# Kernel tuning notes

Hardware: AMD Instinct MI355X
Metric: run time of the kernel (lower is better)

The kernel has to match this reference:

```python
import jax, jax.numpy as jnp
import numpy as np
import math

B, S, D = 4, 1024, 1024
H, DK = 16, 64
NUM_BUCKETS, MAX_DIST = 32, 128


def _relative_position_bucket(relative_position, num_buckets=NUM_BUCKETS, max_distance=MAX_DIST):
    # bidirectional bucketing (T5 encoder style)
    num_buckets = num_buckets // 2
    buckets = (relative_position > 0).astype(jnp.int32) * num_buckets
    rp = jnp.abs(relative_position)
    max_exact = num_buckets // 2
    is_small = rp < max_exact
    # clamp to >=1 to avoid log(0); masked out by is_small anyway
    rp_large = max_exact + (
        jnp.log(jnp.maximum(rp, 1).astype(jnp.float32) / max_exact)
        / math.log(max_distance / max_exact)
        * (num_buckets - max_exact)
    ).astype(jnp.int32)
    rp_large = jnp.minimum(rp_large, num_buckets - 1)
    return buckets + jnp.where(is_small, rp, rp_large)


def compute_bias(rel_bias_table, q_len, k_len):
    ctx = jnp.arange(q_len)[:, None]
    mem = jnp.arange(k_len)[None, :]
    buckets = _relative_position_bucket(mem - ctx)  # [q,k]
    values = rel_bias_table[buckets]  # [q,k,H]
    return jnp.transpose(values, (2, 0, 1))  # [H,q,k]


def setup_inputs() -> dict:
    key = jax.random.key(0)
    ks = jax.random.split(key, 6)
    return {
        "hidden_states": jax.random.normal(ks[0], (B, S, D), dtype=jnp.float32),
        "Wq": jax.random.normal(ks[1], (D, H * DK), dtype=jnp.float32) * 0.02,
        "Wk": jax.random.normal(ks[2], (D, H * DK), dtype=jnp.float32) * 0.02,
        "Wv": jax.random.normal(ks[3], (D, H * DK), dtype=jnp.float32) * 0.02,
        "Wo": jax.random.normal(ks[4], (H * DK, D), dtype=jnp.float32) * 0.02,
        "rel_bias_table": jax.random.normal(ks[5], (NUM_BUCKETS, H), dtype=jnp.float32),
    }


def reference(hidden_states, Wq, Wk, Wv, Wo, rel_bias_table):
    b, s, _ = hidden_states.shape
    # projections (no bias), split heads -> [b,h,s,dk]
    def heads(x):
        return jnp.transpose(x.reshape(b, s, H, DK), (0, 2, 1, 3))
    q = heads(hidden_states @ Wq)
    k = heads(hidden_states @ Wk)
    v = heads(hidden_states @ Wv)
    # NOTE: T5 attention is UNSCALED (no 1/sqrt(dk))
    scores = jnp.einsum("bhqd,bhkd->bhqk", q, k)
    bias = compute_bias(rel_bias_table, s, s)[None]  # [1,H,s,s]
    scores = scores + bias
    attn = jax.nn.softmax(scores.astype(jnp.float32), axis=-1).astype(scores.dtype)
    out = jnp.einsum("bhqk,bhkd->bhqd", attn, v)
    out = jnp.transpose(out, (0, 2, 1, 3)).reshape(b, s, H * DK)
    return out @ Wo
```

## Files before the change

### kernel.cpp

```cpp
#include <hip/hip_runtime.h>
#include <hip/hip_bf16.h>

typedef __attribute__((ext_vector_type(8))) short short8;
typedef __attribute__((ext_vector_type(4))) float f32x4;
typedef __attribute__((ext_vector_type(4))) unsigned u32x4;
typedef unsigned short u16;

#define AS1 __attribute__((address_space(1)))
#define AS3 __attribute__((address_space(3)))

#define LOG2E 1.44269504088896f
#define FOLD_M 46.166241308446828f
#define EXP2(x) __builtin_amdgcn_exp2f(x)
#define WAITV(n) asm volatile("s_waitcnt vmcnt(" #n ")" ::: "memory")

__device__ __forceinline__ u16 f2bf(float f) {
    unsigned u = __builtin_bit_cast(unsigned, f);
    u += 0x7FFFu + ((u >> 16) & 1u);
    return (u16)(u >> 16);
}

__device__ __forceinline__ unsigned pk2(float a, float b) {
    unsigned ua = __builtin_bit_cast(unsigned, a) + 0x8000u;
    unsigned ub = __builtin_bit_cast(unsigned, b) + 0x8000u;
    return __builtin_amdgcn_perm(ub, ua, 0x07060302);
}

__global__ __launch_bounds__(256) void k_prep(const float* __restrict__ hidden,
                                              const float* __restrict__ Wq, const float* __restrict__ Wk,
                                              const float* __restrict__ Wv, const float* __restrict__ Wo,
                                              const float* __restrict__ tbl,
                                              u16* __restrict__ hidb,
                                              u16* __restrict__ wt, u16* __restrict__ wot,
                                              float* __restrict__ bias2) {
    int z = blockIdx.z;
    if (z >= 5) {
        int i = ((z - 5) * 1024 + blockIdx.y * 32 + blockIdx.x) * 256 + threadIdx.x;
        float4 v = ((const float4*)hidden)[i];
        ushort4 o;
        o.x = f2bf(v.x); o.y = f2bf(v.y); o.z = f2bf(v.z); o.w = f2bf(v.w);
        ((ushort4*)hidb)[i] = o;
        return;
    }
    if (z == 4) {
        int idx = (blockIdx.y * 32 + blockIdx.x) * 256 + threadIdx.x;
        if (idx < 16 * 2048) {
            int r = idx & 2047, h = idx >> 11;
            int rel = r - 1023;
            int bucket = rel > 0 ? 16 : 0;
            int rp = rel < 0 ? -rel : rel;
            if (rp < 8) bucket += rp;
            else {
                int lb = 8 + (int)(log2f((float)rp * 0.125f) * 2.0f);
                bucket += (lb < 15 ? lb : 15);
            }
            bias2[idx] = tbl[bucket * 16 + h] * LOG2E - FOLD_M;
        }
        return;
    }
    const float* in = z == 0 ? Wq : z == 1 ? Wk : z == 2 ? Wv : Wo;
    u16* out = (z == 3) ? wot : wt + (size_t)z * 1024 * 1024;
    __shared__ float tile[32][33];
    int tx = threadIdx.x & 31, ty = threadIdx.x >> 5;
    int bx = blockIdx.x << 5, by = blockIdx.y << 5;
    #pragma unroll
    for (int j = 0; j < 32; j += 8)
        tile[ty + j][tx] = in[(size_t)(by + ty + j) * 1024 + bx + tx];
    __syncthreads();
    #pragma unroll
    for (int j = 0; j < 32; j += 8)
        out[(size_t)(bx + ty + j) * 1024 + by + tx] = f2bf(tile[tx][ty + j]);
}

template<int MODE, int FM>
__global__ __launch_bounds__(256) void k_gemm(const u16* __restrict__ A, const u16* __restrict__ Bt,
                                              u16* __restrict__ oq, u16* __restrict__ ok,
                                              u16* __restrict__ ov, float* __restrict__ outf,
                                              int N) {
    const int K = 1024;
    const int GX = (MODE == 0) ? 24 : 8;
    const int NWG = (MODE == 0) ? 768 : 512;
    __shared__ __align__(16) u16 As[3][FM * 1024];
    __shared__ __align__(16) u16 Bs[3][4096];
    int t = threadIdx.x, lane = t & 63, wave = t >> 6;
    int bid = blockIdx.y * GX + blockIdx.x;
    int sbid = (bid & 7) * (NWG / 8) + (bid >> 3);
    int m0 = (sbid / GX) * (FM * 32), n0 = (sbid % GX) << 7;
    int wm = (wave >> 1) * (FM * 16), wn = (wave & 1) << 6;
    int g = lane >> 4, ln = lane & 15;
    f32x4 acc[FM][4];
    #pragma unroll
    for (int i = 0; i < FM; i++)
        #pragma unroll
        for (int j = 0; j < 4; j++) acc[i][j] = (f32x4){0.f, 0.f, 0.f, 0.f};

    int schunk = ((lane & 3) ^ ((lane >> 3) & 3)) << 3;
    const u16* gA = A + (size_t)(m0 + wave * 16 + (lane >> 2)) * K + schunk;
    const u16* gB = Bt + (size_t)(n0 + wave * 16 + (lane >> 2)) * K + schunk;
    int ldsOff = wave * 512;

    #define GSTAGE(k0_, buf_)                                                                          \
        {                                                                                              \
            u16* sA = &As[buf_][0];                                                                    \
            u16* sB = &Bs[buf_][0];                                                                    \
            __builtin_amdgcn_global_load_lds((const AS1 void*)(gA + (k0_)),                            \
                                             (AS3 void*)&sA[ldsOff], 16, 0, 0);                        \
            if (FM == 4)                                                                               \
                __builtin_amdgcn_global_load_lds((const AS1 void*)(gA + 64 * K + (k0_)),               \
                                                 (AS3 void*)&sA[ldsOff + 2048], 16, 0, 0);             \
            __builtin_amdgcn_global_load_lds((const AS1 void*)(gB + (k0_)),                            \
                                             (AS3 void*)&sB[ldsOff], 16, 0, 0);                        \
            __builtin_amdgcn_global_load_lds((const AS1 void*)(gB + 64 * K + (k0_)),                   \
                                             (AS3 void*)&sB[ldsOff + 2048], 16, 0, 0);                 \
        }

    GSTAGE(0, 0);
    GSTAGE(32, 1);

    int rchunk = (g ^ ((ln >> 1) & 3)) << 3;
    int c0 = 0, c2 = 2;

    for (int kb = 0; kb < 32; kb++) {
        if (kb < 30) {
            GSTAGE((kb + 2) * 32, c2);
            if (FM == 4) WAITV(8); else WAITV(6);
        } else if (kb == 30) {
            if (FM == 4) WAITV(4); else WAITV(3);
        } else {
            WAITV(0);
        }
        __builtin_amdgcn_s_barrier();

        const u16* rA = &As[c0][0];
        const u16* rB = &Bs[c0][0];
        short8 af[FM], bfr[4];
        #pragma unroll
        for (int fm = 0; fm < FM; fm++)
            af[fm] = *(const short8*)&rA[(wm + (fm << 4) + ln) * 32 + rchunk];
        #pragma unroll
        for (int fn = 0; fn < 4; fn++)
            bfr[fn] = *(const short8*)&rB[(wn + (fn << 4) + ln) * 32 + rchunk];
        __builtin_amdgcn_s_setprio(1);
        #pragma unroll
        for (int fm = 0; fm < FM; fm++)
            #pragma unroll
            for (int fn = 0; fn < 4; fn++)
                acc[fm][fn] = __builtin_amdgcn_mfma_f32_16x16x32_bf16(af[fm], bfr[fn], acc[fm][fn], 0, 0, 0);
        __builtin_amdgcn_s_setprio(0);
        __builtin_amdgcn_s_barrier();

        int old = c0;
        c0 = (c0 == 2) ? 0 : c0 + 1;
        c2 = old;
    }

    #pragma unroll
    for (int fm = 0; fm < FM; fm++)
        #pragma unroll
        for (int fn = 0; fn < 4; fn++) {
            int mb = m0 + wm + (fm << 4) + (g << 2);
            int n = n0 + wn + (fn << 4) + ln;
            if (MODE == 0) {
                int j = n >> 10, col = n & 1023;
                int h = col >> 6, dk = col & 63;
                int b = mb >> 10, s = mb & 1023;
                if (j == 2) {
                    ushort4 pk;
                    pk.x = f2bf(acc[fm][fn][0]); pk.y = f2bf(acc[fm][fn][1]);
                    pk.z = f2bf(acc[fm][fn][2]); pk.w = f2bf(acc[fm][fn][3]);
                    *(ushort4*)(ov + ((size_t)(((b << 4) + h) * 64 + dk)) * 1024 + s) = pk;
                } else {
                    u16* dst = (j == 0) ? oq : ok;
                    #pragma unroll
                    for (int r = 0; r < 4; r++)
                        dst[((size_t)(((b << 4) + h) * 1024 + s + r)) * 64 + dk] = f2bf(acc[fm][fn][r]);
                }
            } else {
                #pragma unroll
                for (int r = 0; r < 4; r++)
                    outf[(size_t)(mb + r) * N + n] = acc[fm][fn][r];
            }
        }
    #undef GSTAGE
}

__global__ __launch_bounds__(256, 2) void k_attn(const u16* __restrict__ Qg, const u16* __restrict__ Kg,
                                                 const u16* __restrict__ Vtg, const float* __restrict__ bias2,
                                                 u16* __restrict__ attn_out) {
    __shared__ __align__(16) u16 Ks[2][64 * 64];
    __shared__ __align__(16) u16 Vts[2][64 * 64];
    __shared__ __align__(16) float blds4[4][1160];

    int t = threadIdx.x, lane = t & 63, w = t >> 6;
    int bid = blockIdx.x;
    int sid = (bid & 7) * 64 + (bid >> 3);
    int qb = sid & 7, h = (sid >> 3) & 15, b = sid >> 7;
    int q0 = qb << 7;
    const u16* Qh = Qg + ((size_t)(((b << 4) + h) * 1024 + q0)) * 64;
    const u16* Kh = Kg + (size_t)(((b << 4) + h)) * 1024 * 64;
    const u16* Vth = Vtg + (size_t)(((b << 4) + h)) * 64 * 1024;
    const float* bh = bias2 + (h << 11);

    int g = lane >> 4, ln = lane & 15;
    int lnk = (ln & 3) | ((ln & 4) << 1) | ((ln & 8) >> 1);
    int kbq = ((g & 1) << 3) | ((g >> 1) << 2);

    short8 qf[2][2];
    #pragma unroll
    for (int fm = 0; fm < 2; fm++)
        #pragma unroll
        for (int kh = 0; kh < 2; kh++)
            qf[fm][kh] = *(const short8*)(Qh + (size_t)(w * 32 + fm * 16 + ln) * 64 + kh * 32 + g * 8);

    int w0 = 896 - q0;
    for (int i = t; i < 1152; i += 256) {
        float v = bh[w0 + i];
        #pragma unroll
        for (int a2 = 0; a2 < 4; a2++) { int x = i - a2; if (x >= 0) blds4[a2][x] = v; }
    }
    float b_hi = bh[1023 + 256];
    float b_lo = bh[1023 - 256];
    int aRep = (3 - ln) & 3;
    const float* repB = &blds4[aRep][0];

    #define STAGE(kb_, buf_)                                                                     \
        {                                                                                        \
            _Pragma("unroll")                                                                    \
            for (int r2 = 0; r2 < 2; r2++) {                                                     \
                int L = t * 16 + r2 * 4096;                                                      \
                int row = L >> 7, gI = (L >> 4) & 7, gp = gI ^ (row & 7);                        \
                __builtin_amdgcn_global_load_lds(                                                \
                    (const AS1 void*)(Kh + (size_t)((kb_) * 64 + row) * 64 + gp * 8),            \
                    (AS3 void*)&Ks[buf_][L >> 1], 16, 0, 0);                                     \
                __builtin_amdgcn_global_load_lds(                                                \
                    (const AS1 void*)(Vth + (size_t)row * 1024 + (kb_) * 64 + gp * 8),           \
                    (AS3 void*)&Vts[buf_][L >> 1], 16, 0, 0);                                    \
            }                                                                                    \
        }

    STAGE(0, 0);
    __syncthreads();

    float psum[2] = {0.f, 0.f};
    f32x4 o[2][4];
    #pragma unroll
    for (int fm = 0; fm < 2; fm++)
        #pragma unroll
        for (int dn = 0; dn < 4; dn++) o[fm][dn] = (f32x4){0.f, 0.f, 0.f, 0.f};

    #pragma unroll 2
    for (int kb = 0; kb < 16; kb++) {
        const int cur = kb & 1;
        if (kb < 15) STAGE(kb + 1, cur ^ 1);

        f32x4 s[2][4];
        __builtin_amdgcn_s_setprio(1);
        #pragma unroll
        for (int fn = 0; fn < 4; fn++) {
            int row = (fn << 4) + lnk;
            short8 kf0 = *(const short8*)((const char*)Ks[cur] + row * 128 + (((g << 4) + 0)  ^ ((row & 7) << 4)));
            short8 kf1 = *(const short8*)((const char*)Ks[cur] + row * 128 + (((g << 4) + 64) ^ ((row & 7) << 4)));
            #pragma unroll
            for (int fm = 0; fm < 2; fm++) {
                f32x4 a = (f32x4){0.f, 0.f, 0.f, 0.f};
                a = __builtin_amdgcn_mfma_f32_16x16x32_bf16(kf0, qf[fm][0], a, 0, 0, 0);
                a = __builtin_amdgcn_mfma_f32_16x16x32_bf16(kf1, qf[fm][1], a, 0, 0, 0);
                s[fm][fn] = a;
            }
        }
        __builtin_amdgcn_s_setprio(0);

        int d0 = 64 * kb - q0 - 32 * w;
        int ibase = 64 * kb - 32 * w + 127 + kbq - ln;
        bool fast = (d0 >= 122) || (d0 <= -154);
        float bu = d0 > 0 ? b_hi : b_lo;
        unsigned Px[2][4], Py[2][4];
        #pragma unroll
        for (int fm = 0; fm < 2; fm++)
            #pragma unroll
            for (int fn = 0; fn < 4; fn++) {
                f32x4 sv = s[fm][fn];
                float b0, b1, b2v, b3;
                if (fast) { b0 = b1 = b2v = b3 = bu; }
                else {
                    float4 bb = *(const float4*)(repB + (ibase + 16 * fn - 16 * fm - aRep));
                    b0 = bb.x; b1 = bb.y; b2v = bb.z; b3 = bb.w;
                }
                float p0 = EXP2(fmaf(sv[0], LOG2E, b0));
                float p1 = EXP2(fmaf(sv[1], LOG2E, b1));
                float p2 = EXP2(fmaf(sv[2], LOG2E, b2v));
                float p3 = EXP2(fmaf(sv[3], LOG2E, b3));
                psum[fm] += (p0 + p1) + (p2 + p3);
                Px[fm][fn] = pk2(p0, p1);
                Py[fm][fn] = pk2(p2, p3);
            }

        short8 pa[2][2];
        #pragma unroll
        for (int fm = 0; fm < 2; fm++)
            #pragma unroll
            for (int ks = 0; ks < 2; ks++) {
                unsigned w0r = Px[fm][2 * ks], w2r = Px[fm][2 * ks + 1];
                unsigned w1r = Py[fm][2 * ks], w3r = Py[fm][2 * ks + 1];
                asm volatile("s_nop 1\n\tv_permlane32_swap_b32 %0, %1" : "+v"(w0r), "+v"(w2r));
                asm volatile("s_nop 1\n\tv_permlane32_swap_b32 %0, %1" : "+v"(w1r), "+v"(w3r));
                u32x4 tv; tv[0] = w0r; tv[1] = w1r; tv[2] = w2r; tv[3] = w3r;
                pa[fm][ks] = __builtin_bit_cast(short8, tv);
            }

        __builtin_amdgcn_s_setprio(1);
        #pragma unroll
        for (int dn = 0; dn < 4; dn++) {
            int vrow = (dn << 4) + ln;
            short8 vb0 = *(const short8*)((const char*)Vts[cur] + vrow * 128 + (((g << 4) + 0)  ^ ((vrow & 7) << 4)));
            short8 vb1 = *(const short8*)((const char*)Vts[cur] + vrow * 128 + (((g << 4) + 64) ^ ((vrow & 7) << 4)));
            #pragma unroll
            for (int fm = 0; fm < 2; fm++) {
                f32x4 a = o[fm][dn];
                a = __builtin_amdgcn_mfma_f32_16x16x32_bf16(pa[fm][0], vb0, a, 0, 0, 0);
                a = __builtin_amdgcn_mfma_f32_16x16x32_bf16(pa[fm][1], vb1, a, 0, 0, 0);
                o[fm][dn] = a;
            }
        }
        __builtin_amdgcn_s_setprio(0);

        __syncthreads();
    }

    float linv[2][4];
    #pragma unroll
    for (int fm = 0; fm < 2; fm++) {
        float v = psum[fm];
        v += __shfl_xor(v, 16);
        v += __shfl_xor(v, 32);
        float inv = 1.0f / v;
        #pragma unroll
        for (int r = 0; r < 4; r++)
            linv[fm][r] = __shfl(inv, 4 * g + r);
    }
    #pragma unroll
    for (int fm = 0; fm < 2; fm++)
        #pragma unroll
        for (int dn = 0; dn < 4; dn++)
            #pragma unroll
            for (int r = 0; r < 4; r++) {
                int srow = q0 + 32 * w + 16 * fm + (g << 2) + r;
                int col = (h << 6) + (dn << 4) + ln;
                attn_out[((size_t)((b << 10) + srow) << 10) + col] = f2bf(o[fm][dn][r] * linv[fm][r]);
            }
}

extern "C" void kernel_launch(void* const* d_in, const int* in_sizes, int n_in,
                              void* d_out, int out_size, void* d_ws, size_t ws_size,
                              hipStream_t stream) {
    const float* hidden = (const float*)d_in[0];
    const float* Wq = (const float*)d_in[1];
    const float* Wk = (const float*)d_in[2];
    const float* Wv = (const float*)d_in[3];
    const float* Wo = (const float*)d_in[4];
    const float* tbl = (const float*)d_in[5];

    u16* hidb = (u16*)d_ws;
    u16* wt   = hidb + 4096 * 1024;
    u16* wot  = wt + 3072 * 1024;
    u16* Qb   = wot + 1024 * 1024;
    u16* Kb   = Qb + 4 * 16 * 1024 * 64;
    u16* Vb   = Kb + 4 * 16 * 1024 * 64;
    u16* attn = Vb + 4 * 16 * 1024 * 64;
    float* bias = (float*)(attn + 4096 * 1024);

    k_prep<<<dim3(32, 32, 9), 256, 0, stream>>>(hidden, Wq, Wk, Wv, Wo, tbl, hidb, wt, wot, bias);
    k_gemm<0, 4><<<dim3(24, 32), 256, 0, stream>>>(hidb, wt, Qb, Kb, Vb, nullptr, 3072);
    k_attn<<<512, 256, 0, stream>>>(Qb, Kb, Vb, bias, attn);
    k_gemm<1, 2><<<dim3(8, 64), 256, 0, stream>>>(attn, wot, nullptr, nullptr, nullptr,
                                                  (float*)d_out, 1024);
}
```

Before: 97.24 us.

## Replace QKV projection GEMM with 256x192-tile 512-thread kernel

The fused QKV projection now uses a dedicated kernel with 256x192 output tiles, 8 waves per block, BK=64 double-buffered LDS staging with XOR swizzle, and an XCD-aware tile mapping giving 256 blocks, one per CU. Larger tiles raise arithmetic intensity and cut redundant global/LDS traffic compared with the old 128x128 tile template. The output projection is split into its own non-templated kernel with unchanged behaviour. Risks are higher register pressure from 24 accumulators per wave and a single wave of blocks with no tail balancing.

After: 95.88 us. About the same (-1.4%).

```diff
diff --git a/kernel.cpp b/kernel.cpp
--- a/kernel.cpp
+++ b/kernel.cpp
@@ -72,25 +72,118 @@
         out[(size_t)(bx + ty + j) * 1024 + by + tx] = f2bf(tile[tx][ty + j]);
 }
 
-template<int MODE, int FM>
-__global__ __launch_bounds__(256) void k_gemm(const u16* __restrict__ A, const u16* __restrict__ Bt,
-                                              u16* __restrict__ oq, u16* __restrict__ ok,
-                                              u16* __restrict__ ov, float* __restrict__ outf,
-                                              int N) {
-    const int K = 1024;
-    const int GX = (MODE == 0) ? 24 : 8;
-    const int NWG = (MODE == 0) ? 768 : 512;
-    __shared__ __align__(16) u16 As[3][FM * 1024];
+__global__ __launch_bounds__(512, 2) void k_qkv(const u16* __restrict__ A, const u16* __restrict__ Bt,
+                                                u16* __restrict__ oq, u16* __restrict__ ok,
+                                                u16* __restrict__ ov) {
+    __shared__ __align__(16) u16 As[2][256 * 64];
+    __shared__ __align__(16) u16 Bs[2][192 * 64];
+    int t = threadIdx.x, lane = t & 63, wave = t >> 6;
+    int g = lane >> 4, ln = lane & 15;
+    int wr = wave >> 2, wc = wave & 3;
+
+    int bid = blockIdx.x;
+    int xcd = bid & 7, wgl = bid >> 3;
+    int mt = ((xcd & 3) << 2) + (wgl >> 3);
+    int nt = ((xcd >> 2) << 3) + (wgl & 7);
+    int m0 = mt << 8, n0 = nt * 192;
+
+    f32x4 acc[8][3];
+    #pragma unroll
+    for (int i = 0; i < 8; i++)
+        #pragma unroll
+        for (int j = 0; j < 3; j++) acc[i][j] = (f32x4){0.f, 0.f, 0.f, 0.f};
+
+    #define QSTG(kt_, buf_)                                                                      \
+        {                                                                                        \
+            _Pragma("unroll")                                                                    \
+            for (int u = 0; u < 4; u++) {                                                        \
+                int L = t * 16 + u * 8192;                                                       \
+                int row = L >> 7, gI = (L >> 4) & 7, gp = gI ^ (row & 7);                        \
+                __builtin_amdgcn_global_load_lds(                                                \
+                    (const AS1 void*)(A + (size_t)(m0 + row) * 1024 + (kt_) * 64 + gp * 8),      \
+                    (AS3 void*)&As[buf_][L >> 1], 16, 0, 0);                                     \
+            }                                                                                    \
+            _Pragma("unroll")                                                                    \
+            for (int u = 0; u < 3; u++) {                                                        \
+                int L = t * 16 + u * 8192;                                                       \
+                int row = L >> 7, gI = (L >> 4) & 7, gp = gI ^ (row & 7);                        \
+                __builtin_amdgcn_global_load_lds(                                                \
+                    (const AS1 void*)(Bt + (size_t)(n0 + row) * 1024 + (kt_) * 64 + gp * 8),     \
+                    (AS3 void*)&Bs[buf_][L >> 1], 16, 0, 0);                                     \
+            }                                                                                    \
+        }
+
+    QSTG(0, 0);
+    __syncthreads();
+
+    #pragma unroll 2
+    for (int kt = 0; kt < 16; kt++) {
+        const int c = kt & 1;
+        if (kt < 15) QSTG(kt + 1, c ^ 1);
+
+        #pragma unroll
+        for (int ks = 0; ks < 2; ks++) {
+            short8 af[8], bfr[3];
+            int cb = ((ks << 2) + g) << 4;
+            #pragma unroll
+            for (int mf = 0; mf < 8; mf++) {
+                int row = (wr << 7) + (mf << 4) + ln;
+                af[mf] = *(const short8*)((const char*)&As[c][0] + row * 128 + (cb ^ ((row & 7) << 4)));
+            }
+            #pragma unroll
+            for (int nf = 0; nf < 3; nf++) {
+                int row = wc * 48 + (nf << 4) + ln;
+                bfr[nf] = *(const short8*)((const char*)&Bs[c][0] + row * 128 + (cb ^ ((row & 7) << 4)));
+            }
+            __builtin_amdgcn_s_setprio(1);
+            #pragma unroll
+            for (int mf = 0; mf < 8; mf++)
+                #pragma unroll
+                for (int nf = 0; nf < 3; nf++)
+                    acc[mf][nf] = __builtin_amdgcn_mfma_f32_16x16x32_bf16(af[mf], bfr[nf], acc[mf][nf], 0, 0, 0);
+            __builtin_amdgcn_s_setprio(0);
+        }
+        __syncthreads();
+    }
+    #undef QSTG
+
+    #pragma unroll
+    for (int mf = 0; mf < 8; mf++)
+        #pragma unroll
+        for (int nf = 0; nf < 3; nf++) {
+            int mb = m0 + (wr << 7) + (mf << 4) + (g << 2);
+            int n = n0 + wc * 48 + (nf << 4) + ln;
+            int j = n >> 10, col = n & 1023;
+            int h = col >> 6, dk = col & 63;
+            int b = mb >> 10, s = mb & 1023;
+            if (j == 2) {
+                ushort4 pk;
+                pk.x = f2bf(acc[mf][nf][0]); pk.y = f2bf(acc[mf][nf][1]);
+                pk.z = f2bf(acc[mf][nf][2]); pk.w = f2bf(acc[mf][nf][3]);
+                *(ushort4*)(ov + ((size_t)(((b << 4) + h) * 64 + dk)) * 1024 + s) = pk;
+            } else {
+                u16* dst = (j == 0) ? oq : ok;
+                #pragma unroll
+                for (int r = 0; r < 4; r++)
+                    dst[((size_t)(((b << 4) + h) * 1024 + s + r)) * 64 + dk] = f2bf(acc[mf][nf][r]);
+            }
+        }
+}
+
+__global__ __launch_bounds__(256) void k_gemm_out(const u16* __restrict__ A, const u16* __restrict__ Bt,
+                                                  float* __restrict__ outf) {
+    const int K = 1024, N = 1024;
+    __shared__ __align__(16) u16 As[3][2048];
     __shared__ __align__(16) u16 Bs[3][4096];
     int t = threadIdx.x, lane = t & 63, wave = t >> 6;
-    int bid = blockIdx.y * GX + blockIdx.x;
-    int sbid = (bid & 7) * (NWG / 8) + (bid >> 3);
-    int m0 = (sbid / GX) * (FM * 32), n0 = (sbid % GX) << 7;
-    int wm = (wave >> 1) * (FM * 16), wn = (wave & 1) << 6;
+    int bid = blockIdx.y * 8 + blockIdx.x;
+    int sbid = (bid & 7) * 64 + (bid >> 3);
+    int m0 = (sbid / 8) * 64, n0 = (sbid % 8) << 7;
+    int wm = (wave >> 1) * 32, wn = (wave & 1) << 6;
     int g = lane >> 4, ln = lane & 15;
-    f32x4 acc[FM][4];
-    #pragma unroll
-    for (int i = 0; i < FM; i++)
+    f32x4 acc[2][4];
+    #pragma unroll
+    for (int i = 0; i < 2; i++)
         #pragma unroll
         for (int j = 0; j < 4; j++) acc[i][j] = (f32x4){0.f, 0.f, 0.f, 0.f};
 
@@ -105,9 +198,6 @@
             u16* sB = &Bs[buf_][0];                                                                    \
             __builtin_amdgcn_global_load_lds((const AS1 void*)(gA + (k0_)),                            \
                                              (AS3 void*)&sA[ldsOff], 16, 0, 0);                        \
-            if (FM == 4)                                                                               \
-                __builtin_amdgcn_global_load_lds((const AS1 void*)(gA + 64 * K + (k0_)),               \
-                                                 (AS3 void*)&sA[ldsOff + 2048], 16, 0, 0);             \
             __builtin_amdgcn_global_load_lds((const AS1 void*)(gB + (k0_)),                            \
                                              (AS3 void*)&sB[ldsOff], 16, 0, 0);                        \
             __builtin_amdgcn_global_load_lds((const AS1 void*)(gB + 64 * K + (k0_)),                   \
@@ -123,9 +213,9 @@
     for (int kb = 0; kb < 32; kb++) {
         if (kb < 30) {
             GSTAGE((kb + 2) * 32, c2);
-            if (FM == 4) WAITV(8); else WAITV(6);
+            WAITV(6);
         } else if (kb == 30) {
-            if (FM == 4) WAITV(4); else WAITV(3);
+            WAITV(3);
         } else {
             WAITV(0);
         }
@@ -133,16 +223,16 @@
 
         const u16* rA = &As[c0][0];
         const u16* rB = &Bs[c0][0];
-        short8 af[FM], bfr[4];
-        #pragma unroll
-        for (int fm = 0; fm < FM; fm++)
+        short8 af[2], bfr[4];
+        #pragma unroll
+        for (int fm = 0; fm < 2; fm++)
             af[fm] = *(const short8*)&rA[(wm + (fm << 4) + ln) * 32 + rchunk];
         #pragma unroll
         for (int fn = 0; fn < 4; fn++)
             bfr[fn] = *(const short8*)&rB[(wn + (fn << 4) + ln) * 32 + rchunk];
         __builtin_amdgcn_s_setprio(1);
         #pragma unroll
-        for (int fm = 0; fm < FM; fm++)
+        for (int fm = 0; fm < 2; fm++)
             #pragma unroll
             for (int fn = 0; fn < 4; fn++)
                 acc[fm][fn] = __builtin_amdgcn_mfma_f32_16x16x32_bf16(af[fm], bfr[fn], acc[fm][fn], 0, 0, 0);
@@ -155,31 +245,14 @@
     }
 
     #pragma unroll
-    for (int fm = 0; fm < FM; fm++)
+    for (int fm = 0; fm < 2; fm++)
         #pragma unroll
         for (int fn = 0; fn < 4; fn++) {
             int mb = m0 + wm + (fm << 4) + (g << 2);
             int n = n0 + wn + (fn << 4) + ln;
-            if (MODE == 0) {
-                int j = n >> 10, col = n & 1023;
-                int h = col >> 6, dk = col & 63;
-                int b = mb >> 10, s = mb & 1023;
-                if (j == 2) {
-                    ushort4 pk;
-                    pk.x = f2bf(acc[fm][fn][0]); pk.y = f2bf(acc[fm][fn][1]);
-                    pk.z = f2bf(acc[fm][fn][2]); pk.w = f2bf(acc[fm][fn][3]);
-                    *(ushort4*)(ov + ((size_t)(((b << 4) + h) * 64 + dk)) * 1024 + s) = pk;
-                } else {
-                    u16* dst = (j == 0) ? oq : ok;
-                    #pragma unroll
-                    for (int r = 0; r < 4; r++)
-                        dst[((size_t)(((b << 4) + h) * 1024 + s + r)) * 64 + dk] = f2bf(acc[fm][fn][r]);
-                }
-            } else {
-                #pragma unroll
-                for (int r = 0; r < 4; r++)
-                    outf[(size_t)(mb + r) * N + n] = acc[fm][fn][r];
-            }
+            #pragma unroll
+            for (int r = 0; r < 4; r++)
+                outf[(size_t)(mb + r) * N + n] = acc[fm][fn][r];
         }
     #undef GSTAGE
 }
@@ -370,8 +443,7 @@
     float* bias = (float*)(attn + 4096 * 1024);
 
     k_prep<<<dim3(32, 32, 9), 256, 0, stream>>>(hidden, Wq, Wk, Wv, Wo, tbl, hidb, wt, wot, bias);
-    k_gemm<0, 4><<<dim3(24, 32), 256, 0, stream>>>(hidb, wt, Qb, Kb, Vb, nullptr, 3072);
+    k_qkv<<<256, 512, 0, stream>>>(hidb, wt, Qb, Kb, Vb);
     k_attn<<<512, 256, 0, stream>>>(Qb, Kb, Vb, bias, attn);
-    k_gemm<1, 2><<<dim3(8, 64), 256, 0, stream>>>(attn, wot, nullptr, nullptr, nullptr,
-                                                  (float*)d_out, 1024);
-}
+    k_gemm_out<<<dim3(8, 64), 256, 0, stream>>>(attn, wot, (float*)d_out);
+}
```
